# Kernel tuning notes

Measured on AMD Instinct MI355X. Metric: run time of the kernel, lower is better.

## Reference

```python
import jax, jax.numpy as jnp
import numpy as np

N = 100000
F_IN = 256
F_OUT = 64
E = 3200000
NEG_SLOPE = 0.2


def setup_inputs() -> dict:
    key = jax.random.key(0)
    k1, k2, k3, k4, k5 = jax.random.split(key, 5)
    x = jax.random.normal(k1, (N, F_IN), dtype=jnp.float32)
    edge_index = jax.random.randint(k2, (2, E), 0, N, dtype=jnp.int32)
    # GATConv params (heads=1): lin weight, att_src, att_dst, bias
    W = jax.random.normal(k3, (F_IN, F_OUT), dtype=jnp.float32) / np.sqrt(F_IN)
    att_src = jax.random.normal(k4, (F_OUT,), dtype=jnp.float32) / np.sqrt(F_OUT)
    att_dst = jax.random.normal(k5, (F_OUT,), dtype=jnp.float32) / np.sqrt(F_OUT)
    bias = jnp.zeros((F_OUT,), dtype=jnp.float32)
    return {"x": x, "edge_index": edge_index, "W": W,
            "att_src": att_src, "att_dst": att_dst, "bias": bias}


def reference(x, edge_index, W, att_src, att_dst, bias):
    n = x.shape[0]
    h = x @ W  # [N, F_OUT]
    # add self-loops (PyG default add_self_loops=True)
    loops = jnp.arange(n, dtype=edge_index.dtype)
    src = jnp.concatenate([edge_index[0], loops])  # message source j
    dst = jnp.concatenate([edge_index[1], loops])  # message target i
    # per-node attention halves
    a_src = h @ att_src  # [N]
    a_dst = h @ att_dst  # [N]
    e = a_src[src] + a_dst[dst]  # [E+N]
    e = jnp.where(e > 0, e, NEG_SLOPE * e)  # LeakyReLU(0.2)
    # softmax over edges grouped by target node
    e_max = jax.ops.segment_max(e, dst, num_segments=n)
    e_max = jnp.where(jnp.isfinite(e_max), e_max, 0.0)
    p = jnp.exp(e - e_max[dst])
    denom = jax.ops.segment_sum(p, dst, num_segments=n)
    alpha = p / (denom[dst] + 1e-16)  # [E+N]
    # scatter-aggregate weighted source features
    out = jax.ops.segment_sum(alpha[:, None] * h[src], dst, num_segments=n)
    return out + bias
```

## Files before the change

kernel.cpp:

```cpp
#include <hip/hip_runtime.h>
#include <hip/hip_bf16.h>
#include <math.h>

#define F_IN 256
#define F_OUT 64
#define NEG_SLOPE 0.2f
#define SHIFT 7
#define NPB 128
#define MAXK 1024
#define CAP 4608
#define OVF 4
#define GRID_B 256

__device__ __forceinline__ float bf2f(__hip_bfloat16 v) {
    return __bfloat162float(v);
}

typedef short short8 __attribute__((ext_vector_type(8)));
typedef float f32x4 __attribute__((ext_vector_type(4)));

__device__ __forceinline__ unsigned int bf16_bits(float v) {
    unsigned int u = __float_as_uint(v);
    return (u + 0x7fffu + ((u >> 16) & 1u)) >> 16;
}

#define WHI(q, c, l) (((((q)*4 + (c)) * 64) + (l)) * 8)
#define WLO(q, c, l) (16384 + WHI(q, c, l))

__global__ __launch_bounds__(512, 2) void gemm_kernel(
    const float* __restrict__ x, const float* __restrict__ W,
    const float* __restrict__ att_src, const float* __restrict__ att_dst,
    __hip_bfloat16* __restrict__ h16, float* __restrict__ a_src,
    float* __restrict__ a_dst, int N, int nTiles)
{
    __shared__ unsigned short sW[32768];

    const int t = threadIdx.x;
    const int lane = t & 63;
    const int w = t >> 6;
    const int g = lane >> 4;
    const int fr = lane & 15;

    for (int idx = t; idx < 2048; idx += 512) {
        const int q = idx >> 8;
        const int c = (idx >> 6) & 3;
        const int l = idx & 63;
        const int col = c * 16 + (l & 15);
        const float* wp = W + (size_t)(q * 32 + ((l >> 4) * 8)) * F_OUT + col;
        short8 hv, lv;
#pragma unroll
        for (int e = 0; e < 8; e++) {
            float wv = wp[(size_t)e * F_OUT];
            unsigned int hb = bf16_bits(wv);
            float hf = __uint_as_float(hb << 16);
            unsigned int lb = bf16_bits(wv - hf);
            hv[e] = (short)hb;
            lv[e] = (short)lb;
        }
        *(short8*)&sW[WHI(q, c, l)] = hv;
        *(short8*)&sW[WLO(q, c, l)] = lv;
    }
    __syncthreads();

    float as4[4], ad4[4];
#pragma unroll
    for (int c = 0; c < 4; c++) {
        as4[c] = att_src[c * 16 + fr];
        ad4[c] = att_dst[c * 16 + fr];
    }

    const float4 z4 = make_float4(0.f, 0.f, 0.f, 0.f);

    for (int tile = blockIdx.x; tile < nTiles; tile += gridDim.x) {
        const int R0 = tile * 128 + w * 16;
        const int rowA = R0 + fr;
        const bool okA = rowA < N;
        const float* xrow = x + (size_t)rowA * F_IN + g * 8;

        f32x4 acc[4];
#pragma unroll
        for (int c = 0; c < 4; c++) acc[c] = (f32x4){0.f, 0.f, 0.f, 0.f};

        float4 cur0 = okA ? *(const float4*)(xrow + 0) : z4;
        float4 cur1 = okA ? *(const float4*)(xrow + 4) : z4;

#pragma unroll
        for (int q = 0; q < 8; q++) {
            float4 nxt0 = z4, nxt1 = z4;
            if (q < 7) {
                nxt0 = okA ? *(const float4*)(xrow + (q + 1) * 32)     : z4;
                nxt1 = okA ? *(const float4*)(xrow + (q + 1) * 32 + 4) : z4;
            }

            const float vf[8] = {cur0.x, cur0.y, cur0.z, cur0.w,
                                 cur1.x, cur1.y, cur1.z, cur1.w};
            short8 ahi, alo;
#pragma unroll
            for (int e = 0; e < 8; e++) {
                unsigned int hb = bf16_bits(vf[e]);
                float hf = __uint_as_float(hb << 16);
                unsigned int lb = bf16_bits(vf[e] - hf);
                ahi[e] = (short)hb;
                alo[e] = (short)lb;
            }
#pragma unroll
            for (int c = 0; c < 4; c++) {
                short8 bh = *(const short8*)&sW[WHI(q, c, lane)];
                short8 bl = *(const short8*)&sW[WLO(q, c, lane)];
                acc[c] = __builtin_amdgcn_mfma_f32_16x16x32_bf16(ahi, bh, acc[c], 0, 0, 0);
                acc[c] = __builtin_amdgcn_mfma_f32_16x16x32_bf16(alo, bh, acc[c], 0, 0, 0);
                acc[c] = __builtin_amdgcn_mfma_f32_16x16x32_bf16(ahi, bl, acc[c], 0, 0, 0);
            }
            cur0 = nxt0;
            cur1 = nxt1;
            __builtin_amdgcn_sched_barrier(0);
        }

        float sr[4] = {0.f, 0.f, 0.f, 0.f};
        float sd[4] = {0.f, 0.f, 0.f, 0.f};
#pragma unroll
        for (int c = 0; c < 4; c++) {
#pragma unroll
            for (int r = 0; r < 4; r++) {
                float v = acc[c][r];
                sr[r] = fmaf(v, as4[c], sr[r]);
                sd[r] = fmaf(v, ad4[c], sd[r]);
            }
        }
#pragma unroll
        for (int off = 1; off <= 8; off <<= 1) {
#pragma unroll
            for (int r = 0; r < 4; r++) {
                sr[r] += __shfl_xor(sr[r], off, 64);
                sd[r] += __shfl_xor(sd[r], off, 64);
            }
        }

#pragma unroll
        for (int r = 0; r < 4; r++) {
            const int row = R0 + g * 4 + r;
            if (row < N) {
                unsigned int lo = bf16_bits(acc[0][r]) | (bf16_bits(acc[1][r]) << 16);
                unsigned int hi = bf16_bits(acc[2][r]) | (bf16_bits(acc[3][r]) << 16);
                *(int2*)(h16 + (size_t)row * F_OUT + fr * 4) = make_int2((int)lo, (int)hi);
            }
        }

        if (fr < 4) {
            const int row = R0 + g * 4 + fr;
            if (row < N) {
                float vs = (fr == 0) ? sr[0] : (fr == 1) ? sr[1] : (fr == 2) ? sr[2] : sr[3];
                float vd = (fr == 0) ? sd[0] : (fr == 1) ? sd[1] : (fr == 2) ? sd[2] : sd[3];
                a_src[row] = vs;
                a_dst[row] = vd;
            }
        }
    }
}

__global__ __launch_bounds__(1024) void bucket_count_kernel(
    const int* __restrict__ dst, int* __restrict__ pbh, int E, int K, int R)
{
    __shared__ int s[MAXK];
    const int t = threadIdx.x;
    for (int b = t; b < K; b += 1024) s[b] = 0;
    __syncthreads();
    const int start = blockIdx.x * R;
    const int end = min(E, start + R);
    for (int e = start + t * 4; e < end; e += 4096) {
        if (e + 3 < end) {
            int4 d = *(const int4*)&dst[e];
            atomicAdd(&s[d.x >> SHIFT], 1);
            atomicAdd(&s[d.y >> SHIFT], 1);
            atomicAdd(&s[d.z >> SHIFT], 1);
            atomicAdd(&s[d.w >> SHIFT], 1);
        } else {
            for (int q = e; q < end; q++) atomicAdd(&s[dst[q] >> SHIFT], 1);
        }
    }
    __syncthreads();
    int* row = pbh + (size_t)blockIdx.x * K;
    for (int b = t; b < K; b += 1024) row[b] = s[b];
}

__global__ __launch_bounds__(64) void colscan_kernel(
    const int* __restrict__ pbh, int* __restrict__ cbase,
    int* __restrict__ btot, int K, int NBLK)
{
    const int k = blockIdx.x;
    const int lane = threadIdx.x;
    int v[4];
#pragma unroll
    for (int c = 0; c < 4; c++) {
        int b = c * 64 + lane;
        v[c] = (b < NBLK) ? pbh[(size_t)b * K + k] : 0;
    }
    int carry = 0;
#pragma unroll
    for (int c = 0; c < 4; c++) {
        int orig = v[c];
        int s = v[c];
#pragma unroll
        for (int off = 1; off < 64; off <<= 1) {
            int u = __shfl_up(s, off, 64);
            if (lane >= off) s += u;
        }
        int b = c * 64 + lane;
        if (b < NBLK) cbase[(size_t)b * K + k] = carry + s - orig;
        carry += __shfl(s, 63, 64);
    }
    if (lane == 0) btot[k] = carry;
}

__global__ __launch_bounds__(1024) void bbase_scan_kernel(
    const int* __restrict__ btot, int* __restrict__ bbase, int K, int E)
{
    __shared__ int s[1024];
    const int t = threadIdx.x;
    int v = (t < K) ? btot[t] : 0;
    s[t] = v;
    __syncthreads();
    for (int off = 1; off < 1024; off <<= 1) {
        int u = (t >= off) ? s[t - off] : 0;
        __syncthreads();
        s[t] += u;
        __syncthreads();
    }
    if (t < K) bbase[t] = s[t] - v;
    if (t == 0) bbase[K] = E;
}

__global__ __launch_bounds__(1024) void bin_kernel(
    const int* __restrict__ ei, const int* __restrict__ cbase,
    const int* __restrict__ bbase, int* __restrict__ rec, int E, int K, int R)
{
    __shared__ int cb[MAXK];
    const int t = threadIdx.x;
    const int start = blockIdx.x * R;
    const int end = min(E, start + R);
    const int* crow = cbase + (size_t)blockIdx.x * K;
    for (int b = t; b < K; b += 1024) cb[b] = bbase[b] + crow[b];
    __syncthreads();

    for (int e = start + t * 4; e < end; e += 4096) {
        if (e + 3 < end) {
            int4 jj = *(const int4*)&ei[e];
            int4 ii = *(const int4*)&ei[E + e];
            int p0 = atomicAdd(&cb[ii.x >> SHIFT], 1);
            int p1 = atomicAdd(&cb[ii.y >> SHIFT], 1);
            int p2 = atomicAdd(&cb[ii.z >> SHIFT], 1);
            int p3 = atomicAdd(&cb[ii.w >> SHIFT], 1);
            rec[p0] = jj.x | ((ii.x & (NPB - 1)) << 17);
            rec[p1] = jj.y | ((ii.y & (NPB - 1)) << 17);
            rec[p2] = jj.z | ((ii.z & (NPB - 1)) << 17);
            rec[p3] = jj.w | ((ii.w & (NPB - 1)) << 17);
        } else {
            for (int q = e; q < end; q++) {
                int j = ei[q], i = ei[E + q];
                int pos = atomicAdd(&cb[i >> SHIFT], 1);
                rec[pos] = j | ((i & (NPB - 1)) << 17);
            }
        }
    }
}

__global__ __launch_bounds__(256) void sort_kernel(
    int* __restrict__ rec, const int* __restrict__ bbase,
    int* __restrict__ row_ptr, int N, int E, int K)
{
    __shared__ int stage[CAP];
    __shared__ int deg[NPB];
    __shared__ int sval[NPB];
    __shared__ int base[NPB];
    __shared__ int cnt[NPB];
    const int t = threadIdx.x;
    const int b = blockIdx.x;
    const int s = bbase[b], e = bbase[b + 1];
    const int tot = e - s;
    const int nodeBase = b << SHIFT;
    const int nodes = min(NPB, N - nodeBase);

    if (t < NPB) deg[t] = 0;
    __syncthreads();

    int ovf[OVF];
    for (int r = t; r < tot; r += 256) {
        int m = rec[s + r];
        if (r < CAP) stage[r] = m;
        else { int k = (r - CAP) >> 8; if (k < OVF) ovf[k] = m; }
        atomicAdd(&deg[(m >> 17) & (NPB - 1)], 1);
    }
    __syncthreads();

    if (t < NPB) sval[t] = deg[t];
    __syncthreads();
    for (int off = 1; off < NPB; off <<= 1) {
        int v = (t < NPB && t >= off) ? sval[t - off] : 0;
        __syncthreads();
        if (t < NPB) sval[t] += v;
        __syncthreads();
    }
    if (t < NPB) {
        base[t] = sval[t] - deg[t];
        cnt[t] = 0;
        if (t < nodes) row_ptr[nodeBase + t] = s + base[t];
    }
    if (b == K - 1 && t == 0) row_ptr[N] = E;
    __syncthreads();

    for (int r = t; r < tot; r += 256) {
        int m = (r < CAP) ? stage[r] : ovf[(r - CAP) >> 8];
        int li = (m >> 17) & (NPB - 1);
        int rk = atomicAdd(&cnt[li], 1);
        rec[s + base[li] + rk] = m;
    }
}

__global__ __launch_bounds__(256) void node_kernel(
    const __hip_bfloat16* __restrict__ h16, const float* __restrict__ a_src,
    const float* __restrict__ a_dst, const int* __restrict__ row_ptr,
    const int* __restrict__ rec, const float* __restrict__ bias,
    float* __restrict__ out, int N)
{
    __shared__ int   sj[4][64];
    __shared__ float sp[4][64];

    const int w = threadIdx.x >> 6;
    const int lane = threadIdx.x & 63;
    const int i = blockIdx.x * 4 + w;
    if (i >= N) return;

    const int q = lane >> 4;
    const int a = lane & 15;
    const unsigned short* __restrict__ hb = (const unsigned short*)h16;
    const unsigned short* __restrict__ hba = hb + a * 4;

    int*   sjw = &sj[w][0];
    float* spw = &sp[w][0];
    const int*   sjq = &sj[w][q];
    const float* spq = &sp[w][q];

    const int s = row_ptr[i];
    const int e = row_ptr[i + 1];

    const float adst_i = a_dst[i];
    float vs = a_src[i] + adst_i;
    vs = fmaxf(vs, NEG_SLOPE * vs);
    const float pself = __expf(vs);
    float denl = (lane == 0) ? pself : 0.f;

    float acc0 = 0.f, acc1 = 0.f, acc2 = 0.f, acc3 = 0.f;

    for (int k = s; k < e; k += 64) {
        const int cnt = min(64, e - k);
        const int G = (cnt + 3) >> 2;
        int r = (lane < cnt) ? rec[k + lane] : 0;
        int j = r & 0x1FFFF;
        sjw[lane] = j;

        float asj = a_src[j];
        __builtin_amdgcn_sched_barrier(0);

        int2 d[16];
#pragma unroll
        for (int g = 0; g < 16; g++) {
            if (g < G) {
                int jsel = sjq[4 * g];
                d[g] = *(const int2*)(hba + (size_t)jsel * F_OUT);
            }
        }

        float v = asj + adst_i;
        v = fmaxf(v, NEG_SLOPE * v);
        float p = __expf(v);
        if (lane >= cnt) p = 0.f;
        denl += p;
        spw[lane] = p;
        __builtin_amdgcn_sched_barrier(0);

#pragma unroll
        for (int g = 0; g < 16; g++) {
            if (g < G) {
                float psel = spq[4 * g];
                unsigned int lo = (unsigned int)d[g].x;
                unsigned int hi = (unsigned int)d[g].y;
                acc0 = fmaf(psel, __uint_as_float(lo << 16), acc0);
                acc1 = fmaf(psel, __uint_as_float(lo & 0xFFFF0000u), acc1);
                acc2 = fmaf(psel, __uint_as_float(hi << 16), acc2);
                acc3 = fmaf(psel, __uint_as_float(hi & 0xFFFF0000u), acc3);
            }
        }
        __builtin_amdgcn_sched_barrier(0);
    }

#pragma unroll
    for (int o = 16; o <= 32; o <<= 1) {
        acc0 += __shfl_xor(acc0, o, 64);
        acc1 += __shfl_xor(acc1, o, 64);
        acc2 += __shfl_xor(acc2, o, 64);
        acc3 += __shfl_xor(acc3, o, 64);
    }
    float den = denl;
#pragma unroll
    for (int o = 32; o > 0; o >>= 1) den += __shfl_xor(den, o, 64);
    den += 1e-16f;

    if (lane < 16) {
        int2 hs = *(const int2*)(hb + (size_t)i * F_OUT + a * 4);
        unsigned int lo = (unsigned int)hs.x, hi = (unsigned int)hs.y;
        float s0 = acc0 + pself * __uint_as_float(lo << 16);
        float s1 = acc1 + pself * __uint_as_float(lo & 0xFFFF0000u);
        float s2 = acc2 + pself * __uint_as_float(hi << 16);
        float s3 = acc3 + pself * __uint_as_float(hi & 0xFFFF0000u);
        float* orow = out + (size_t)i * F_OUT;
        orow[ 0 + a] = s0 / den + bias[ 0 + a];
        orow[16 + a] = s1 / den + bias[16 + a];
        orow[32 + a] = s2 / den + bias[32 + a];
        orow[48 + a] = s3 / den + bias[48 + a];
    }
}

extern "C" void kernel_launch(void* const* d_in, const int* in_sizes, int n_in,
                              void* d_out, int out_size, void* d_ws, size_t ws_size,
                              hipStream_t stream)
{
    const float* x      = (const float*)d_in[0];
    const int*   ei     = (const int*)d_in[1];
    const float* W      = (const float*)d_in[2];
    const float* att_sr = (const float*)d_in[3];
    const float* att_ds = (const float*)d_in[4];
    const float* bias   = (const float*)d_in[5];
    float* out = (float*)d_out;

    const int N = in_sizes[0] / F_IN;
    const int E = in_sizes[1] / 2;
    const int K = (N + NPB - 1) >> SHIFT;
    const int R = (((E + GRID_B - 1) / GRID_B) + 3) & ~3;

    char* ws = (char*)d_ws;
    size_t off = 0;
    auto alloc = [&](size_t bytes) -> void* {
        void* p = ws + off;
        off = (off + bytes + 255) & ~(size_t)255;
        return p;
    };
    __hip_bfloat16* h16 = (__hip_bfloat16*)alloc((size_t)N * F_OUT * 2);
    float* a_src   = (float*)alloc((size_t)N * 4);
    float* a_dst   = (float*)alloc((size_t)N * 4);
    int*   pbh     = (int*)alloc((size_t)GRID_B * K * 4);
    int*   cbase   = (int*)alloc((size_t)GRID_B * K * 4);
    int*   btot    = (int*)alloc((size_t)K * 4);
    int*   bbase   = (int*)alloc((size_t)(K + 1) * 4);
    int*   row_ptr = (int*)alloc((size_t)(N + 1) * 4);
    int*   rec     = (int*)alloc((size_t)E * 4);
    (void)ws_size; (void)n_in; (void)out_size;

    const int nTiles = (N + 127) >> 7;
    const int gemmGrid = nTiles < 512 ? nTiles : 512;

    gemm_kernel<<<gemmGrid, 512, 0, stream>>>(x, W, att_sr, att_ds, h16, a_src, a_dst, N, nTiles);
    bucket_count_kernel<<<GRID_B, 1024, 0, stream>>>(ei + E, pbh, E, K, R);
    colscan_kernel<<<K, 64, 0, stream>>>(pbh, cbase, btot, K, GRID_B);
    bbase_scan_kernel<<<1, 1024, 0, stream>>>(btot, bbase, K, E);
    bin_kernel<<<GRID_B, 1024, 0, stream>>>(ei, cbase, bbase, rec, E, K, R);
    sort_kernel<<<K, 256, 0, stream>>>(rec, bbase, row_ptr, N, E, K);
    node_kernel<<<(N + 3) / 4, 256, 0, stream>>>(h16, a_src, a_dst, row_ptr, rec, bias, out, N);
}
```

Before: 318.9 us.

## Replace two-level bucket sort with direct per-node counting sort via global atomics

The CSR build no longer uses the bucket count, column scan, bin and in-LDS sort kernels. Instead it counts per-node in-degree with global atomics, runs a three-phase prefix scan to get row_ptr, and scatters source indices straight into their final slots using atomicSub on the degree counters. This cuts the number of passes over the edge list and the staging through buckets. In exchange it relies on contended global atomics and fully random 4-byte scatter writes, and the order of edges within each row becomes nondeterministic.

```diff
diff --git a/kernel.cpp b/kernel.cpp
--- a/kernel.cpp
+++ b/kernel.cpp
@@ -5,12 +5,6 @@
 #define F_IN 256
 #define F_OUT 64
 #define NEG_SLOPE 0.2f
-#define SHIFT 7
-#define NPB 128
-#define MAXK 1024
-#define CAP 4608
-#define OVF 4
-#define GRID_B 256
 
 __device__ __forceinline__ float bf2f(__hip_bfloat16 v) {
     return __bfloat162float(v);
@@ -158,66 +152,48 @@
     }
 }
 
-__global__ __launch_bounds__(1024) void bucket_count_kernel(
-    const int* __restrict__ dst, int* __restrict__ pbh, int E, int K, int R)
-{
-    __shared__ int s[MAXK];
-    const int t = threadIdx.x;
-    for (int b = t; b < K; b += 1024) s[b] = 0;
-    __syncthreads();
-    const int start = blockIdx.x * R;
-    const int end = min(E, start + R);
-    for (int e = start + t * 4; e < end; e += 4096) {
-        if (e + 3 < end) {
-            int4 d = *(const int4*)&dst[e];
-            atomicAdd(&s[d.x >> SHIFT], 1);
-            atomicAdd(&s[d.y >> SHIFT], 1);
-            atomicAdd(&s[d.z >> SHIFT], 1);
-            atomicAdd(&s[d.w >> SHIFT], 1);
-        } else {
-            for (int q = e; q < end; q++) atomicAdd(&s[dst[q] >> SHIFT], 1);
-        }
-    }
-    __syncthreads();
-    int* row = pbh + (size_t)blockIdx.x * K;
-    for (int b = t; b < K; b += 1024) row[b] = s[b];
-}
-
-__global__ __launch_bounds__(64) void colscan_kernel(
-    const int* __restrict__ pbh, int* __restrict__ cbase,
-    int* __restrict__ btot, int K, int NBLK)
-{
-    const int k = blockIdx.x;
-    const int lane = threadIdx.x;
-    int v[4];
-#pragma unroll
-    for (int c = 0; c < 4; c++) {
-        int b = c * 64 + lane;
-        v[c] = (b < NBLK) ? pbh[(size_t)b * K + k] : 0;
-    }
-    int carry = 0;
-#pragma unroll
-    for (int c = 0; c < 4; c++) {
-        int orig = v[c];
-        int s = v[c];
-#pragma unroll
-        for (int off = 1; off < 64; off <<= 1) {
-            int u = __shfl_up(s, off, 64);
-            if (lane >= off) s += u;
-        }
-        int b = c * 64 + lane;
-        if (b < NBLK) cbase[(size_t)b * K + k] = carry + s - orig;
-        carry += __shfl(s, 63, 64);
-    }
-    if (lane == 0) btot[k] = carry;
-}
-
-__global__ __launch_bounds__(1024) void bbase_scan_kernel(
-    const int* __restrict__ btot, int* __restrict__ bbase, int K, int E)
+__global__ __launch_bounds__(1024) void zero_kernel(int* __restrict__ p, int n)
+{
+    const int i = blockIdx.x * 1024 + threadIdx.x;
+    if (i < n) p[i] = 0;
+}
+
+__global__ __launch_bounds__(256) void deg_count_kernel(
+    const int* __restrict__ dst, int* __restrict__ deg, int E)
+{
+    const int e = (blockIdx.x * 256 + threadIdx.x) * 4;
+    if (e + 3 < E) {
+        int4 d = *(const int4*)&dst[e];
+        atomicAdd(&deg[d.x], 1);
+        atomicAdd(&deg[d.y], 1);
+        atomicAdd(&deg[d.z], 1);
+        atomicAdd(&deg[d.w], 1);
+    } else if (e < E) {
+        for (int q = e; q < E; q++) atomicAdd(&deg[dst[q]], 1);
+    }
+}
+
+__global__ __launch_bounds__(1024) void scan_part_kernel(
+    const int* __restrict__ deg, int* __restrict__ psum, int N)
 {
     __shared__ int s[1024];
     const int t = threadIdx.x;
-    int v = (t < K) ? btot[t] : 0;
+    const int i = blockIdx.x * 1024 + t;
+    s[t] = (i < N) ? deg[i] : 0;
+    __syncthreads();
+    for (int off = 512; off > 0; off >>= 1) {
+        if (t < off) s[t] += s[t + off];
+        __syncthreads();
+    }
+    if (t == 0) psum[blockIdx.x] = s[0];
+}
+
+__global__ __launch_bounds__(1024) void scan_base_kernel(
+    int* __restrict__ psum, int P, int* __restrict__ row_ptr, int N, int E)
+{
+    __shared__ int s[1024];
+    const int t = threadIdx.x;
+    int v = (t < P) ? psum[t] : 0;
     s[t] = v;
     __syncthreads();
     for (int off = 1; off < 1024; off <<= 1) {
@@ -226,93 +202,51 @@
         s[t] += u;
         __syncthreads();
     }
-    if (t < K) bbase[t] = s[t] - v;
-    if (t == 0) bbase[K] = E;
-}
-
-__global__ __launch_bounds__(1024) void bin_kernel(
-    const int* __restrict__ ei, const int* __restrict__ cbase,
-    const int* __restrict__ bbase, int* __restrict__ rec, int E, int K, int R)
-{
-    __shared__ int cb[MAXK];
+    if (t < P) psum[t] = s[t] - v;
+    if (t == 0) row_ptr[N] = E;
+}
+
+__global__ __launch_bounds__(1024) void scan_write_kernel(
+    const int* __restrict__ deg, const int* __restrict__ psum,
+    int* __restrict__ row_ptr, int N)
+{
+    __shared__ int s[1024];
     const int t = threadIdx.x;
-    const int start = blockIdx.x * R;
-    const int end = min(E, start + R);
-    const int* crow = cbase + (size_t)blockIdx.x * K;
-    for (int b = t; b < K; b += 1024) cb[b] = bbase[b] + crow[b];
+    const int i = blockIdx.x * 1024 + t;
+    int v = (i < N) ? deg[i] : 0;
+    s[t] = v;
     __syncthreads();
-
-    for (int e = start + t * 4; e < end; e += 4096) {
-        if (e + 3 < end) {
-            int4 jj = *(const int4*)&ei[e];
-            int4 ii = *(const int4*)&ei[E + e];
-            int p0 = atomicAdd(&cb[ii.x >> SHIFT], 1);
-            int p1 = atomicAdd(&cb[ii.y >> SHIFT], 1);
-            int p2 = atomicAdd(&cb[ii.z >> SHIFT], 1);
-            int p3 = atomicAdd(&cb[ii.w >> SHIFT], 1);
-            rec[p0] = jj.x | ((ii.x & (NPB - 1)) << 17);
-            rec[p1] = jj.y | ((ii.y & (NPB - 1)) << 17);
-            rec[p2] = jj.z | ((ii.z & (NPB - 1)) << 17);
-            rec[p3] = jj.w | ((ii.w & (NPB - 1)) << 17);
-        } else {
-            for (int q = e; q < end; q++) {
-                int j = ei[q], i = ei[E + q];
-                int pos = atomicAdd(&cb[i >> SHIFT], 1);
-                rec[pos] = j | ((i & (NPB - 1)) << 17);
-            }
-        }
-    }
-}
-
-__global__ __launch_bounds__(256) void sort_kernel(
-    int* __restrict__ rec, const int* __restrict__ bbase,
-    int* __restrict__ row_ptr, int N, int E, int K)
-{
-    __shared__ int stage[CAP];
-    __shared__ int deg[NPB];
-    __shared__ int sval[NPB];
-    __shared__ int base[NPB];
-    __shared__ int cnt[NPB];
-    const int t = threadIdx.x;
-    const int b = blockIdx.x;
-    const int s = bbase[b], e = bbase[b + 1];
-    const int tot = e - s;
-    const int nodeBase = b << SHIFT;
-    const int nodes = min(NPB, N - nodeBase);
-
-    if (t < NPB) deg[t] = 0;
-    __syncthreads();
-
-    int ovf[OVF];
-    for (int r = t; r < tot; r += 256) {
-        int m = rec[s + r];
-        if (r < CAP) stage[r] = m;
-        else { int k = (r - CAP) >> 8; if (k < OVF) ovf[k] = m; }
-        atomicAdd(&deg[(m >> 17) & (NPB - 1)], 1);
-    }
-    __syncthreads();
-
-    if (t < NPB) sval[t] = deg[t];
-    __syncthreads();
-    for (int off = 1; off < NPB; off <<= 1) {
-        int v = (t < NPB && t >= off) ? sval[t - off] : 0;
+    for (int off = 1; off < 1024; off <<= 1) {
+        int u = (t >= off) ? s[t - off] : 0;
         __syncthreads();
-        if (t < NPB) sval[t] += v;
+        s[t] += u;
         __syncthreads();
     }
-    if (t < NPB) {
-        base[t] = sval[t] - deg[t];
-        cnt[t] = 0;
-        if (t < nodes) row_ptr[nodeBase + t] = s + base[t];
-    }
-    if (b == K - 1 && t == 0) row_ptr[N] = E;
-    __syncthreads();
-
-    for (int r = t; r < tot; r += 256) {
-        int m = (r < CAP) ? stage[r] : ovf[(r - CAP) >> 8];
-        int li = (m >> 17) & (NPB - 1);
-        int rk = atomicAdd(&cnt[li], 1);
-        rec[s + base[li] + rk] = m;
+    if (i < N) row_ptr[i] = psum[blockIdx.x] + s[t] - v;
+}
+
+__global__ __launch_bounds__(256) void bin_direct_kernel(
+    const int* __restrict__ ei, const int* __restrict__ row_ptr,
+    int* __restrict__ deg, int* __restrict__ rec, int E)
+{
+    const int e = (blockIdx.x * 256 + threadIdx.x) * 4;
+    if (e + 3 < E) {
+        int4 jj = *(const int4*)&ei[e];
+        int4 ii = *(const int4*)&ei[E + e];
+        int o0 = atomicSub(&deg[ii.x], 1);
+        int o1 = atomicSub(&deg[ii.y], 1);
+        int o2 = atomicSub(&deg[ii.z], 1);
+        int o3 = atomicSub(&deg[ii.w], 1);
+        rec[row_ptr[ii.x] + o0 - 1] = jj.x;
+        rec[row_ptr[ii.y] + o1 - 1] = jj.y;
+        rec[row_ptr[ii.z] + o2 - 1] = jj.z;
+        rec[row_ptr[ii.w] + o3 - 1] = jj.w;
+    } else if (e < E) {
+        for (int q = e; q < E; q++) {
+            int j = ei[q], i = ei[E + q];
+            int o = atomicSub(&deg[i], 1);
+            rec[row_ptr[i] + o - 1] = j;
+        }
     }
 }
 
@@ -434,8 +368,6 @@
 
     const int N = in_sizes[0] / F_IN;
     const int E = in_sizes[1] / 2;
-    const int K = (N + NPB - 1) >> SHIFT;
-    const int R = (((E + GRID_B - 1) / GRID_B) + 3) & ~3;
 
     char* ws = (char*)d_ws;
     size_t off = 0;
@@ -447,22 +379,23 @@
     __hip_bfloat16* h16 = (__hip_bfloat16*)alloc((size_t)N * F_OUT * 2);
     float* a_src   = (float*)alloc((size_t)N * 4);
     float* a_dst   = (float*)alloc((size_t)N * 4);
-    int*   pbh     = (int*)alloc((size_t)GRID_B * K * 4);
-    int*   cbase   = (int*)alloc((size_t)GRID_B * K * 4);
-    int*   btot    = (int*)alloc((size_t)K * 4);
-    int*   bbase   = (int*)alloc((size_t)(K + 1) * 4);
+    int*   deg     = (int*)alloc((size_t)N * 4);
+    int*   psum    = (int*)alloc((size_t)1024 * 4);
     int*   row_ptr = (int*)alloc((size_t)(N + 1) * 4);
     int*   rec     = (int*)alloc((size_t)E * 4);
     (void)ws_size; (void)n_in; (void)out_size;
 
     const int nTiles = (N + 127) >> 7;
     const int gemmGrid = nTiles < 512 ? nTiles : 512;
-
+    const int edgeGrid = (E + 1023) / 1024;
+    const int P = (N + 1023) >> 10;
+
+    zero_kernel<<<P, 1024, 0, stream>>>(deg, N);
     gemm_kernel<<<gemmGrid, 512, 0, stream>>>(x, W, att_sr, att_ds, h16, a_src, a_dst, N, nTiles);
-    bucket_count_kernel<<<GRID_B, 1024, 0, stream>>>(ei + E, pbh, E, K, R);
-    colscan_kernel<<<K, 64, 0, stream>>>(pbh, cbase, btot, K, GRID_B);
-    bbase_scan_kernel<<<1, 1024, 0, stream>>>(btot, bbase, K, E);
-    bin_kernel<<<GRID_B, 1024, 0, stream>>>(ei, cbase, bbase, rec, E, K, R);
-    sort_kernel<<<K, 256, 0, stream>>>(rec, bbase, row_ptr, N, E, K);
+    deg_count_kernel<<<edgeGrid, 256, 0, stream>>>(ei + E, deg, E);
+    scan_part_kernel<<<P, 1024, 0, stream>>>(deg, psum, N);
+    scan_base_kernel<<<1, 1024, 0, stream>>>(psum, P, row_ptr, N, E);
+    scan_write_kernel<<<P, 1024, 0, stream>>>(deg, psum, row_ptr, N);
+    bin_direct_kernel<<<edgeGrid, 256, 0, stream>>>(ei, row_ptr, deg, rec, E);
     node_kernel<<<(N + 3) / 4, 256, 0, stream>>>(h16, a_src, a_dst, row_ptr, rec, bias, out, N);
 }
```

New measurement: 668.6 us. 2.1x slower.
